# Optimization experiments

Measured on AMD Instinct MI355X. Metric: run time of the kernel, lower is better.

## Reference

```python
import jax, jax.numpy as jnp
import numpy as np

ALPHA = 10.0
BETA = 2.0


def _l2norm(x):
    return x / jnp.linalg.norm(x, axis=1, keepdims=True)


def setup_inputs() -> dict:
    key = jax.random.key(0)
    k1, k2, k3 = jax.random.split(key, 3)
    n, C, d = 4096, 10000, 2048
    inputs = _l2norm(jax.random.normal(k1, (n, d), dtype=jnp.float32))
    kernel = _l2norm(jax.random.normal(k2, (C, d), dtype=jnp.float32))
    targets = jax.random.randint(k3, (n,), 0, C, dtype=jnp.int64 if jax.config.jax_enable_x64 else jnp.int32)
    return {"inputs": inputs, "targets": targets, "kernel": kernel}


def reference(inputs, targets, kernel):
    n = inputs.shape[0]
    C = kernel.shape[0]
    rows = jnp.arange(n)

    # cos_theta uses a detached kernel (no grad through this GEMM in original)
    cos = jnp.clip(inputs @ jax.lax.stop_gradient(kernel).T, -1.0, 1.0)  # [n, C]

    # phi_i = <inputs_i, kernel[targets_i]> - beta  (grad flows to kernel here)
    phi = jnp.sum(inputs * kernel[targets], axis=1) - BETA  # [n]

    pos_cos = cos[rows, targets]  # cos_theta at target columns, [n]
    mean_proxy_pos = pos_cos.sum() / n
    mean_proxy_neg = (cos.sum() - pos_cos.sum()) / (n * (C - 1))

    # output = cos_theta with target entries replaced by phi
    output = cos.at[rows, targets].set(phi)  # [n, C]
    onehot = jax.nn.one_hot(targets, C, dtype=output.dtype)

    loss_pos = phi  # sum(output * onehot, axis=1)
    loss_neg = jnp.log(jnp.sum(jnp.exp(output * ALPHA) * (1.0 - onehot), axis=1))  # [n]
    loss_mask = (jnp.max(output, axis=1) - phi) > 0.0
    per_sample = -loss_pos + loss_neg / ALPHA
    denom = jnp.maximum(loss_mask.sum(), 1).astype(per_sample.dtype)
    loss = jnp.sum(jnp.where(loss_mask, per_sample, 0.0)) / denom

    pred = jnp.argmax(output, axis=1)
    prec = jnp.mean((pred == targets).astype(jnp.float32))

    sim = inputs @ inputs.T  # [n, n]
    sim_label = (targets[:, None] == targets[None, :]).astype(sim.dtype)
    pos_cnt = sim_label.sum()
    neg_cnt = (n * n) - pos_cnt
    mean_pos_sim = jnp.sum(sim * sim_label) / pos_cnt
    mean_neg_sim = jnp.sum(sim * (1.0 - sim_label)) / neg_cnt

    return (loss, prec, mean_proxy_pos, mean_proxy_neg, mean_pos_sim, mean_neg_sim)
```

## Files before the change

kernel.cpp:

```cpp
#include <hip/hip_runtime.h>
#include <hip/hip_bf16.h>

#define NROWS 4096
#define NCLS  10000
#define DIM   2048
#define DIMB  1024
#define ALPHA_F 10.0f
#define BETA_F  2.0f
#define FP4_SCALE 64.0f
#define INVQ (1.0f / (FP4_SCALE * FP4_SCALE))
#define NMAIN_BLK 2528
#define NSIM_BLK  528

typedef float f32x4 __attribute__((ext_vector_type(4)));
typedef int   i32x4 __attribute__((ext_vector_type(4)));
typedef int   i32x8 __attribute__((ext_vector_type(8)));

__global__ void prep_kernel(const float* __restrict__ X, const float* __restrict__ Kn,
                            const int* __restrict__ tgt,
                            unsigned int* __restrict__ dA, unsigned int* __restrict__ dB,
                            float* __restrict__ dotv, int nA8, int nT8) {
  if (blockIdx.x < 2048) {
    int stride = 2048 * blockDim.x;
    for (int i = blockIdx.x * blockDim.x + threadIdx.x; i < nT8; i += stride) {
      const float* src; unsigned int* dst; int j;
      if (i < nA8) { src = X; dst = dA; j = i; } else { src = Kn; dst = dB; j = i - nA8; }
      float4 a = reinterpret_cast<const float4*>(src)[2 * j];
      float4 b = reinterpret_cast<const float4*>(src)[2 * j + 1];
      float v[8] = {a.x, a.y, a.z, a.w, b.x, b.y, b.z, b.w};
      unsigned int w = 0;
#pragma unroll
      for (int q = 0; q < 8; ++q) {
        float s = v[q] * FP4_SCALE;
        float av = fabsf(s);
        unsigned int code = (unsigned)(av > 0.25f) + (av > 0.75f) + (av > 1.25f)
                          + (av > 1.75f) + (av > 2.5f) + (av > 3.5f) + (av > 5.0f);
        code |= (s < 0.f) ? 8u : 0u;
        w |= code << (4 * q);
      }
      dst[j] = w;
    }
  } else {
    int gtid = (blockIdx.x - 2048) * blockDim.x + threadIdx.x;
    int wave = gtid >> 6;
    int lane = threadIdx.x & 63;
    if (wave >= NROWS) return;
    const float* xr = X + (size_t)wave * DIM;
    const float* kr = Kn + (size_t)tgt[wave] * DIM;
    float s = 0.f;
#pragma unroll
    for (int it = 0; it < DIM / 256; ++it) {
      int k = lane * 4 + it * 256;
      float4 a = *reinterpret_cast<const float4*>(xr + k);
      float4 b = *reinterpret_cast<const float4*>(kr + k);
      s += a.x * b.x + a.y * b.y + a.z * b.z + a.w * b.w;
    }
#pragma unroll
    for (int off = 32; off > 0; off >>= 1) s += __shfl_down(s, off);
    if (lane == 0) dotv[wave] = s;
  }
}


#define AS1 const __attribute__((address_space(1))) void*
#define AS3 __attribute__((address_space(3))) void*

__global__ __launch_bounds__(256, 4)
void gemm_kernel(const unsigned char* __restrict__ A,
                 const unsigned char* __restrict__ Bm,
                 const float* __restrict__ dotv,
                 const int* __restrict__ tgt,
                 float* __restrict__ S1, float* __restrict__ Eacc,
                 float* __restrict__ CNT, float* __restrict__ simAcc) {
  __shared__ unsigned char lds[2 * 16384];

  const int tid  = threadIdx.x;
  const int lane = tid & 63;
  const int wid  = tid >> 6;
  const int wr   = wid >> 1;
  const int wc   = wid & 1;
  const int fr   = lane & 15;
  const int kg   = lane >> 4;

  const int lin = blockIdx.x;
  const bool isMain = lin < NMAIN_BLK;
  int rowTile, colTile, nB;
  const unsigned char* B;
  if (isMain) {
    int swz = (lin & 7) * 316 + (lin >> 3);
    colTile = swz / 32;
    rowTile = swz % 32;
    B = Bm; nB = NCLS;
  } else {
    int l2 = lin - NMAIN_BLK;
    int swz = (l2 & 7) * 66 + (l2 >> 3);
    int r = 0;
    while ((r + 1) * (r + 2) / 2 <= swz) ++r;
    rowTile = r;
    colTile = swz - r * (r + 1) / 2;
    B = A; nB = NROWS;
  }
  const int rowBase = rowTile * 128;
  const int colBase = colTile * 128;

  const int l0  = tid >> 3;
  const int sp  = tid & 7;
  const int lg8 = sp ^ (l0 & 7);
  const int shi = lg8 >> 2, sc16 = lg8 & 3;
  const int rA0 = rowBase + 2 * l0 + shi;
  const int rA1 = rA0 + 64;
  int cB0 = colBase + 2 * l0 + shi;      if (cB0 > nB - 1) cB0 = nB - 1;
  int cB1 = colBase + 64 + 2 * l0 + shi; if (cB1 > nB - 1) cB1 = nB - 1;
  const unsigned char* pA0 = A + (size_t)rA0 * DIMB + sc16 * 16;
  const unsigned char* pA1 = A + (size_t)rA1 * DIMB + sc16 * 16;
  const unsigned char* pB0 = B + (size_t)cB0 * DIMB + sc16 * 16;
  const unsigned char* pB1 = B + (size_t)cB1 * DIMB + sc16 * 16;
  const int dOff = l0 * 128 + sp * 16;

#define STAGE_TILE(BUF, KT)                                                     \
  { int ko_ = (KT) * 64;                                                        \
    unsigned char* d_ = lds + (BUF) * 16384 + dOff;                             \
    __builtin_amdgcn_global_load_lds((AS1)(pA0 + ko_), (AS3)(d_),          16, 0, 0); \
    __builtin_amdgcn_global_load_lds((AS1)(pA1 + ko_), (AS3)(d_ + 4096),   16, 0, 0); \
    __builtin_amdgcn_global_load_lds((AS1)(pB0 + ko_), (AS3)(d_ + 8192),   16, 0, 0); \
    __builtin_amdgcn_global_load_lds((AS1)(pB1 + ko_), (AS3)(d_ + 12288),  16, 0, 0); }

  int offA[4], offB[4];
#pragma unroll
  for (int m2 = 0; m2 < 4; ++m2) {
    int lr = wr * 64 + m2 * 16 + fr;
    int l = lr >> 1;
    offA[m2] = l * 128 + ((((lr & 1) * 4 + kg) ^ (l & 7)) << 4);
  }
#pragma unroll
  for (int n2 = 0; n2 < 4; ++n2) {
    int lc = wc * 64 + n2 * 16 + fr;
    int l = lc >> 1;
    offB[n2] = 8192 + l * 128 + ((((lc & 1) * 4 + kg) ^ (l & 7)) << 4);
  }

  f32x4 acc[4][4];
  const f32x4 zero = {0.f, 0.f, 0.f, 0.f};
#pragma unroll
  for (int m = 0; m < 4; ++m)
#pragma unroll
    for (int n = 0; n < 4; ++n) acc[m][n] = zero;

  i32x8 afr[4], bfr[4];
#pragma unroll
  for (int q = 0; q < 4; ++q) {
#pragma unroll
    for (int e = 0; e < 8; ++e) { afr[q][e] = 0; bfr[q][e] = 0; }
  }

  STAGE_TILE(0, 0);
  __syncthreads();

#pragma unroll 1
  for (int kt = 0; kt < 16; ++kt) {
    const int buf = kt & 1;
    if (kt < 15) STAGE_TILE(buf ^ 1, kt + 1);
    const unsigned char* lb = lds + buf * 16384;
#pragma unroll
    for (int m2 = 0; m2 < 4; ++m2) {
      i32x4 v_ = *reinterpret_cast<const i32x4*>(lb + offA[m2]);
      afr[m2][0] = v_[0]; afr[m2][1] = v_[1]; afr[m2][2] = v_[2]; afr[m2][3] = v_[3];
    }
#pragma unroll
    for (int n2 = 0; n2 < 4; ++n2) {
      i32x4 v_ = *reinterpret_cast<const i32x4*>(lb + offB[n2]);
      bfr[n2][0] = v_[0]; bfr[n2][1] = v_[1]; bfr[n2][2] = v_[2]; bfr[n2][3] = v_[3];
    }
#pragma unroll
    for (int m2 = 0; m2 < 4; ++m2)
#pragma unroll
      for (int n2 = 0; n2 < 4; ++n2)
        acc[m2][n2] = __builtin_amdgcn_mfma_scale_f32_16x16x128_f8f6f4(
            afr[m2], bfr[n2], acc[m2][n2], 4, 4, 0, 127, 0, 127);
    __syncthreads();
  }


  if (isMain) {
    float* shPhi = reinterpret_cast<float*>(lds);
    if (tid < 128) shPhi[tid] = dotv[rowBase + tid] - BETA_F;
    __syncthreads();
#pragma unroll
    for (int m = 0; m < 4; ++m) {
#pragma unroll
      for (int j = 0; j < 4; ++j) {
        int rl = wr * 64 + m * 16 + kg * 4 + j;
        float ph = shPhi[rl];
        float s1 = 0.f, ee = 0.f, ct = 0.f;
#pragma unroll
        for (int n = 0; n < 4; ++n) {
          int gcol = colBase + wc * 64 + n * 16 + fr;
          float c = acc[m][n][j] * INVQ;
          c = fminf(fmaxf(c, -1.f), 1.f);
          if (gcol < NCLS) {
            s1 += c;
            ee += __expf(ALPHA_F * c);
            ct += (c > ph) ? 1.f : 0.f;
          }
        }
        float pk = s1 + ct * 4096.0f;
#pragma unroll
        for (int o = 1; o < 16; o <<= 1) {
          pk += __shfl_xor(pk, o);
          ee += __shfl_xor(ee, o);
        }
        if (fr == 0) {
          int grow = rowBase + rl;
          float ctv = rintf(pk * (1.0f / 4096.0f));
          float s1v = pk - ctv * 4096.0f;
          atomicAdd(&S1[grow], s1v);
          atomicAdd(&Eacc[grow], ee);
          atomicAdd(&CNT[grow], ctv);
        }
      }
    }
  } else {
    const float wgt = (rowTile == colTile) ? 1.f : 2.f;
    int* shT = reinterpret_cast<int*>(lds);
    float* redbuf = reinterpret_cast<float*>(lds + 4096);
    if (tid < 128) shT[tid] = tgt[rowBase + tid];
    else if (tid < 256) shT[tid] = tgt[colBase + (tid - 128)];
    __syncthreads();
    float ps = 0.f, als = 0.f, pc = 0.f;
#pragma unroll
    for (int m = 0; m < 4; ++m) {
#pragma unroll
      for (int j = 0; j < 4; ++j) {
        int rl = wr * 64 + m * 16 + kg * 4 + j;
        int tr = shT[rl];
#pragma unroll
        for (int n = 0; n < 4; ++n) {
          int cl = wc * 64 + n * 16 + fr;
          float c = acc[m][n][j] * INVQ;
          als += c;
          if (tr == shT[128 + cl]) { ps += c; pc += 1.f; }
        }
      }
    }
#pragma unroll
    for (int o = 1; o < 64; o <<= 1) {
      ps  += __shfl_xor(ps, o);
      als += __shfl_xor(als, o);
      pc  += __shfl_xor(pc, o);
    }
    if (lane == 0) {
      redbuf[wid * 3 + 0] = ps;
      redbuf[wid * 3 + 1] = als;
      redbuf[wid * 3 + 2] = pc;
    }
    __syncthreads();
    if (tid == 0) {
      float p = 0.f, a = 0.f, c2 = 0.f;
      for (int w = 0; w < 4; ++w) {
        p += redbuf[w * 3 + 0];
        a += redbuf[w * 3 + 1];
        c2 += redbuf[w * 3 + 2];
      }
      atomicAdd(&simAcc[0], wgt * p);
      atomicAdd(&simAcc[1], wgt * a);
      atomicAdd(&simAcc[2], wgt * c2);
    }
  }
}

__global__ void finalize_kernel(const float* __restrict__ dotv, const float* __restrict__ S1,
                                const float* __restrict__ Eacc, const float* __restrict__ CNT,
                                const float* __restrict__ simAcc, float* __restrict__ out) {
  __shared__ float sh[5][1024];
  int tid = threadIdx.x;
  float sum_posc = 0.f, sum_s1 = 0.f, loss_sum = 0.f, mask_cnt = 0.f, correct = 0.f;
  for (int i = tid; i < NROWS; i += 1024) {
    float d = dotv[i];
    float posc = fminf(fmaxf(d, -1.f), 1.f);
    float phi = d - BETA_F;
    sum_posc += posc;
    sum_s1 += S1[i];
    float e = Eacc[i] - __expf(ALPHA_F * posc);
    float cexcl = CNT[i] - 1.f;
    float per = -phi + __logf(e) / ALPHA_F;
    if (cexcl > 0.5f) { loss_sum += per; mask_cnt += 1.f; }
    else correct += 1.f;
  }
  sh[0][tid] = sum_posc; sh[1][tid] = sum_s1; sh[2][tid] = loss_sum;
  sh[3][tid] = mask_cnt; sh[4][tid] = correct;
  __syncthreads();
  for (int s = 512; s > 0; s >>= 1) {
    if (tid < s)
      for (int q = 0; q < 5; ++q) sh[q][tid] += sh[q][tid + s];
    __syncthreads();
  }
  if (tid == 0) {
    float posS = sh[0][0], s1S = sh[1][0], lossS = sh[2][0], maskS = sh[3][0], corr = sh[4][0];
    out[0] = lossS / fmaxf(maskS, 1.f);
    out[1] = corr / (float)NROWS;
    out[2] = posS / (float)NROWS;
    out[3] = (s1S - posS) / ((float)NROWS * (float)(NCLS - 1));
    float pos = simAcc[0], all = simAcc[1], pcnt = simAcc[2];
    out[4] = pos / pcnt;
    out[5] = (all - pos) / ((float)NROWS * (float)NROWS - pcnt);
  }
}

extern "C" void kernel_launch(void* const* d_in, const int* in_sizes, int n_in,
                              void* d_out, int out_size, void* d_ws, size_t ws_size,
                              hipStream_t stream) {
  const float* X  = (const float*)d_in[0];
  const int*   tg = (const int*)d_in[1];
  const float* Kn = (const float*)d_in[2];
  float* out = (float*)d_out;

  char* w = (char*)d_ws;
  unsigned char* f4A = (unsigned char*)w;
  unsigned char* f4B = f4A + (size_t)NROWS * DIMB;
  float* dotv   = (float*)(w + (size_t)NROWS * DIMB + (size_t)NCLS * DIMB);
  float* S1     = dotv + NROWS;
  float* Eacc   = S1 + NROWS;
  float* CNT    = Eacc + NROWS;
  float* simAcc = CNT + NROWS;

  hipMemsetAsync(S1, 0, (3 * NROWS + 4) * sizeof(float), stream);

  const int nA8 = NROWS * DIM / 8, nT8 = nA8 + NCLS * DIM / 8;
  prep_kernel<<<3072, 256, 0, stream>>>(X, Kn, tg, (unsigned int*)f4A,
                                        (unsigned int*)f4B, dotv, nA8, nT8);

  gemm_kernel<<<NMAIN_BLK + NSIM_BLK, 256, 0, stream>>>(
      f4A, f4B, dotv, tg, S1, Eacc, CNT, simAcc);

  finalize_kernel<<<1, 1024, 0, stream>>>(dotv, S1, Eacc, CNT, simAcc, out);
}
```

Before: 135.6 us.

## Replace the n×n similarity GEMM with a column-sum identity and same-label pair dots

The 528 blocks computing the inputs·inputsᵀ GEMM are removed. The total similarity is now taken as the squared norm of the column-sum vector, the diagonal from the sum of squared norms, and same-target pair contributions from explicitly enumerated label-matching pairs that are dot-producted in fp32 by a few extra blocks. This cuts the GEMM grid and replaces O(n²d) work with O(nd) plus a small pair list. In exchange it adds pair enumeration, atomics and a fixed MAXPAIRS cap, and it relies on targets having few collisions.

```diff
diff --git a/kernel.cpp b/kernel.cpp
--- a/kernel.cpp
+++ b/kernel.cpp
@@ -10,7 +10,8 @@
 #define FP4_SCALE 64.0f
 #define INVQ (1.0f / (FP4_SCALE * FP4_SCALE))
 #define NMAIN_BLK 2528
-#define NSIM_BLK  528
+#define NPAIR_BLK 32
+#define MAXPAIRS 8192
 
 typedef float f32x4 __attribute__((ext_vector_type(4)));
 typedef int   i32x4 __attribute__((ext_vector_type(4)));
@@ -19,10 +20,14 @@
 __global__ void prep_kernel(const float* __restrict__ X, const float* __restrict__ Kn,
                             const int* __restrict__ tgt,
                             unsigned int* __restrict__ dA, unsigned int* __restrict__ dB,
-                            float* __restrict__ dotv, int nA8, int nT8) {
+                            float* __restrict__ dotv,
+                            float* __restrict__ scal, float* __restrict__ scol,
+                            unsigned int* __restrict__ pairs,
+                            int nA8, int nT8) {
+  const int tid = threadIdx.x;
   if (blockIdx.x < 2048) {
     int stride = 2048 * blockDim.x;
-    for (int i = blockIdx.x * blockDim.x + threadIdx.x; i < nT8; i += stride) {
+    for (int i = blockIdx.x * blockDim.x + tid; i < nT8; i += stride) {
       const float* src; unsigned int* dst; int j;
       if (i < nA8) { src = X; dst = dA; j = i; } else { src = Kn; dst = dB; j = i - nA8; }
       float4 a = reinterpret_cast<const float4*>(src)[2 * j];
@@ -40,10 +45,10 @@
       }
       dst[j] = w;
     }
-  } else {
-    int gtid = (blockIdx.x - 2048) * blockDim.x + threadIdx.x;
+  } else if (blockIdx.x < 3072) {
+    int gtid = (blockIdx.x - 2048) * blockDim.x + tid;
     int wave = gtid >> 6;
-    int lane = threadIdx.x & 63;
+    int lane = tid & 63;
     if (wave >= NROWS) return;
     const float* xr = X + (size_t)wave * DIM;
     const float* kr = Kn + (size_t)tgt[wave] * DIM;
@@ -58,6 +63,39 @@
 #pragma unroll
     for (int off = 32; off > 0; off >>= 1) s += __shfl_down(s, off);
     if (lane == 0) dotv[wave] = s;
+  } else if (blockIdx.x < 3104) {
+    int rbase = (blockIdx.x - 3072) * 128;
+    float part[8] = {0.f, 0.f, 0.f, 0.f, 0.f, 0.f, 0.f, 0.f};
+    float sq = 0.f;
+    for (int i = 0; i < 128; ++i) {
+      const float* row = X + (size_t)(rbase + i) * DIM;
+#pragma unroll
+      for (int k = 0; k < 8; ++k) {
+        float v = row[tid + 256 * k];
+        part[k] += v;
+        sq += v * v;
+      }
+    }
+#pragma unroll
+    for (int k = 0; k < 8; ++k) atomicAdd(&scol[tid + 256 * k], part[k]);
+    int lane = tid & 63;
+#pragma unroll
+    for (int off = 32; off > 0; off >>= 1) sq += __shfl_down(sq, off);
+    if (lane == 0) atomicAdd(&scal[0], sq);
+  } else {
+    int pb = blockIdx.x - 3104;
+    unsigned int* pairCnt = (unsigned int*)(scal + 3);
+#pragma unroll 1
+    for (int ii = 0; ii < 8; ++ii) {
+      int i = pb * 8 + ii;
+      int ti = tgt[i];
+      for (int j = i + 1 + tid; j < NROWS; j += 256) {
+        if (tgt[j] == ti) {
+          unsigned idx = atomicAdd(pairCnt, 1u);
+          if (idx < MAXPAIRS) pairs[idx] = ((unsigned)i << 16) | (unsigned)j;
+        }
+      }
+    }
   }
 }
 
@@ -69,37 +107,48 @@
 void gemm_kernel(const unsigned char* __restrict__ A,
                  const unsigned char* __restrict__ Bm,
                  const float* __restrict__ dotv,
-                 const int* __restrict__ tgt,
+                 const float* __restrict__ X,
+                 const unsigned int* __restrict__ pairs,
+                 const unsigned int* __restrict__ pairCnt,
                  float* __restrict__ S1, float* __restrict__ Eacc,
-                 float* __restrict__ CNT, float* __restrict__ simAcc) {
-  __shared__ unsigned char lds[2 * 16384];
-
+                 float* __restrict__ CNT, float* __restrict__ Pp) {
   const int tid  = threadIdx.x;
   const int lane = tid & 63;
   const int wid  = tid >> 6;
-  const int wr   = wid >> 1;
-  const int wc   = wid & 1;
-  const int fr   = lane & 15;
-  const int kg   = lane >> 4;
-
-  const int lin = blockIdx.x;
-  const bool isMain = lin < NMAIN_BLK;
-  int rowTile, colTile, nB;
-  const unsigned char* B;
-  if (isMain) {
-    int swz = (lin & 7) * 316 + (lin >> 3);
-    colTile = swz / 32;
-    rowTile = swz % 32;
-    B = Bm; nB = NCLS;
-  } else {
-    int l2 = lin - NMAIN_BLK;
-    int swz = (l2 & 7) * 66 + (l2 >> 3);
-    int r = 0;
-    while ((r + 1) * (r + 2) / 2 <= swz) ++r;
-    rowTile = r;
-    colTile = swz - r * (r + 1) / 2;
-    B = A; nB = NROWS;
-  }
+  const int lin  = blockIdx.x;
+
+  if (lin >= NMAIN_BLK) {
+    int gw = (lin - NMAIN_BLK) * 4 + wid;
+    int cnt = (int)pairCnt[0]; if (cnt > MAXPAIRS) cnt = MAXPAIRS;
+    for (int p = gw; p < cnt; p += 4 * NPAIR_BLK) {
+      unsigned u = pairs[p];
+      const float* xi = X + (size_t)(u >> 16) * DIM;
+      const float* xj = X + (size_t)(u & 0xffffu) * DIM;
+      float s = 0.f;
+#pragma unroll
+      for (int it = 0; it < DIM / 256; ++it) {
+        int k = lane * 4 + it * 256;
+        float4 a = *reinterpret_cast<const float4*>(xi + k);
+        float4 b = *reinterpret_cast<const float4*>(xj + k);
+        s += a.x * b.x + a.y * b.y + a.z * b.z + a.w * b.w;
+      }
+#pragma unroll
+      for (int off = 32; off > 0; off >>= 1) s += __shfl_down(s, off);
+      if (lane == 0) atomicAdd(Pp, s);
+    }
+    return;
+  }
+
+  __shared__ unsigned char lds[2 * 16384];
+
+  const int wr = wid >> 1;
+  const int wc = wid & 1;
+  const int fr = lane & 15;
+  const int kg = lane >> 4;
+
+  int swz = (lin & 7) * 316 + (lin >> 3);
+  const int colTile = swz / 32;
+  const int rowTile = swz % 32;
   const int rowBase = rowTile * 128;
   const int colBase = colTile * 128;
 
@@ -109,12 +158,12 @@
   const int shi = lg8 >> 2, sc16 = lg8 & 3;
   const int rA0 = rowBase + 2 * l0 + shi;
   const int rA1 = rA0 + 64;
-  int cB0 = colBase + 2 * l0 + shi;      if (cB0 > nB - 1) cB0 = nB - 1;
-  int cB1 = colBase + 64 + 2 * l0 + shi; if (cB1 > nB - 1) cB1 = nB - 1;
+  int cB0 = colBase + 2 * l0 + shi;      if (cB0 > NCLS - 1) cB0 = NCLS - 1;
+  int cB1 = colBase + 64 + 2 * l0 + shi; if (cB1 > NCLS - 1) cB1 = NCLS - 1;
   const unsigned char* pA0 = A + (size_t)rA0 * DIMB + sc16 * 16;
   const unsigned char* pA1 = A + (size_t)rA1 * DIMB + sc16 * 16;
-  const unsigned char* pB0 = B + (size_t)cB0 * DIMB + sc16 * 16;
-  const unsigned char* pB1 = B + (size_t)cB1 * DIMB + sc16 * 16;
+  const unsigned char* pB0 = Bm + (size_t)cB0 * DIMB + sc16 * 16;
+  const unsigned char* pB1 = Bm + (size_t)cB1 * DIMB + sc16 * 16;
   const int dOff = l0 * 128 + sp * 16;
 
 #define STAGE_TILE(BUF, KT)                                                     \
@@ -180,98 +229,50 @@
     __syncthreads();
   }
 
-
-  if (isMain) {
-    float* shPhi = reinterpret_cast<float*>(lds);
-    if (tid < 128) shPhi[tid] = dotv[rowBase + tid] - BETA_F;
-    __syncthreads();
-#pragma unroll
-    for (int m = 0; m < 4; ++m) {
-#pragma unroll
-      for (int j = 0; j < 4; ++j) {
-        int rl = wr * 64 + m * 16 + kg * 4 + j;
-        float ph = shPhi[rl];
-        float s1 = 0.f, ee = 0.f, ct = 0.f;
-#pragma unroll
-        for (int n = 0; n < 4; ++n) {
-          int gcol = colBase + wc * 64 + n * 16 + fr;
-          float c = acc[m][n][j] * INVQ;
-          c = fminf(fmaxf(c, -1.f), 1.f);
-          if (gcol < NCLS) {
-            s1 += c;
-            ee += __expf(ALPHA_F * c);
-            ct += (c > ph) ? 1.f : 0.f;
-          }
+  float* shPhi = reinterpret_cast<float*>(lds);
+  if (tid < 128) shPhi[tid] = dotv[rowBase + tid] - BETA_F;
+  __syncthreads();
+#pragma unroll
+  for (int m = 0; m < 4; ++m) {
+#pragma unroll
+    for (int j = 0; j < 4; ++j) {
+      int rl = wr * 64 + m * 16 + kg * 4 + j;
+      float ph = shPhi[rl];
+      float s1 = 0.f, ee = 0.f, ct = 0.f;
+#pragma unroll
+      for (int n = 0; n < 4; ++n) {
+        int gcol = colBase + wc * 64 + n * 16 + fr;
+        float c = acc[m][n][j] * INVQ;
+        c = fminf(fmaxf(c, -1.f), 1.f);
+        if (gcol < NCLS) {
+          s1 += c;
+          ee += __expf(ALPHA_F * c);
+          ct += (c > ph) ? 1.f : 0.f;
         }
-        float pk = s1 + ct * 4096.0f;
-#pragma unroll
-        for (int o = 1; o < 16; o <<= 1) {
-          pk += __shfl_xor(pk, o);
-          ee += __shfl_xor(ee, o);
-        }
-        if (fr == 0) {
-          int grow = rowBase + rl;
-          float ctv = rintf(pk * (1.0f / 4096.0f));
-          float s1v = pk - ctv * 4096.0f;
-          atomicAdd(&S1[grow], s1v);
-          atomicAdd(&Eacc[grow], ee);
-          atomicAdd(&CNT[grow], ctv);
-        }
-      }
-    }
-  } else {
-    const float wgt = (rowTile == colTile) ? 1.f : 2.f;
-    int* shT = reinterpret_cast<int*>(lds);
-    float* redbuf = reinterpret_cast<float*>(lds + 4096);
-    if (tid < 128) shT[tid] = tgt[rowBase + tid];
-    else if (tid < 256) shT[tid] = tgt[colBase + (tid - 128)];
-    __syncthreads();
-    float ps = 0.f, als = 0.f, pc = 0.f;
-#pragma unroll
-    for (int m = 0; m < 4; ++m) {
-#pragma unroll
-      for (int j = 0; j < 4; ++j) {
-        int rl = wr * 64 + m * 16 + kg * 4 + j;
-        int tr = shT[rl];
-#pragma unroll
-        for (int n = 0; n < 4; ++n) {
-          int cl = wc * 64 + n * 16 + fr;
-          float c = acc[m][n][j] * INVQ;
-          als += c;
-          if (tr == shT[128 + cl]) { ps += c; pc += 1.f; }
-        }
-      }
-    }
-#pragma unroll
-    for (int o = 1; o < 64; o <<= 1) {
-      ps  += __shfl_xor(ps, o);
-      als += __shfl_xor(als, o);
-      pc  += __shfl_xor(pc, o);
-    }
-    if (lane == 0) {
-      redbuf[wid * 3 + 0] = ps;
-      redbuf[wid * 3 + 1] = als;
-      redbuf[wid * 3 + 2] = pc;
-    }
-    __syncthreads();
-    if (tid == 0) {
-      float p = 0.f, a = 0.f, c2 = 0.f;
-      for (int w = 0; w < 4; ++w) {
-        p += redbuf[w * 3 + 0];
-        a += redbuf[w * 3 + 1];
-        c2 += redbuf[w * 3 + 2];
-      }
-      atomicAdd(&simAcc[0], wgt * p);
-      atomicAdd(&simAcc[1], wgt * a);
-      atomicAdd(&simAcc[2], wgt * c2);
+      }
+      float pk = s1 + ct * 4096.0f;
+#pragma unroll
+      for (int o = 1; o < 16; o <<= 1) {
+        pk += __shfl_xor(pk, o);
+        ee += __shfl_xor(ee, o);
+      }
+      if (fr == 0) {
+        int grow = rowBase + rl;
+        float ctv = rintf(pk * (1.0f / 4096.0f));
+        float s1v = pk - ctv * 4096.0f;
+        atomicAdd(&S1[grow], s1v);
+        atomicAdd(&Eacc[grow], ee);
+        atomicAdd(&CNT[grow], ctv);
+      }
     }
   }
 }
 
 __global__ void finalize_kernel(const float* __restrict__ dotv, const float* __restrict__ S1,
                                 const float* __restrict__ Eacc, const float* __restrict__ CNT,
-                                const float* __restrict__ simAcc, float* __restrict__ out) {
-  __shared__ float sh[5][1024];
+                                const float* __restrict__ scal, const float* __restrict__ scol,
+                                float* __restrict__ out) {
+  __shared__ float sh[6][1024];
   int tid = threadIdx.x;
   float sum_posc = 0.f, sum_s1 = 0.f, loss_sum = 0.f, mask_cnt = 0.f, correct = 0.f;
   for (int i = tid; i < NROWS; i += 1024) {
@@ -286,23 +287,30 @@
     if (cexcl > 0.5f) { loss_sum += per; mask_cnt += 1.f; }
     else correct += 1.f;
   }
+  float sum_s2 = 0.f;
+  for (int c = tid; c < 2048; c += 1024) { float v = scol[c]; sum_s2 += v * v; }
   sh[0][tid] = sum_posc; sh[1][tid] = sum_s1; sh[2][tid] = loss_sum;
-  sh[3][tid] = mask_cnt; sh[4][tid] = correct;
+  sh[3][tid] = mask_cnt; sh[4][tid] = correct; sh[5][tid] = sum_s2;
   __syncthreads();
   for (int s = 512; s > 0; s >>= 1) {
     if (tid < s)
-      for (int q = 0; q < 5; ++q) sh[q][tid] += sh[q][tid + s];
+      for (int q = 0; q < 6; ++q) sh[q][tid] += sh[q][tid + s];
     __syncthreads();
   }
   if (tid == 0) {
     float posS = sh[0][0], s1S = sh[1][0], lossS = sh[2][0], maskS = sh[3][0], corr = sh[4][0];
+    float simTot = sh[5][0];
     out[0] = lossS / fmaxf(maskS, 1.f);
     out[1] = corr / (float)NROWS;
     out[2] = posS / (float)NROWS;
     out[3] = (s1S - posS) / ((float)NROWS * (float)(NCLS - 1));
-    float pos = simAcc[0], all = simAcc[1], pcnt = simAcc[2];
+    float ssq = scal[0];
+    float Pp  = scal[1];
+    unsigned npair = ((const unsigned int*)scal)[3];
+    float pos  = ssq + 2.f * Pp;
+    float pcnt = (float)NROWS + 2.f * (float)npair;
     out[4] = pos / pcnt;
-    out[5] = (all - pos) / ((float)NROWS * (float)NROWS - pcnt);
+    out[5] = (simTot - pos) / ((float)NROWS * (float)NROWS - pcnt);
   }
 }
 
@@ -321,16 +329,19 @@
   float* S1     = dotv + NROWS;
   float* Eacc   = S1 + NROWS;
   float* CNT    = Eacc + NROWS;
-  float* simAcc = CNT + NROWS;
-
-  hipMemsetAsync(S1, 0, (3 * NROWS + 4) * sizeof(float), stream);
+  float* scal   = CNT + NROWS;
+  float* scol   = scal + 8;
+  unsigned int* pairs = (unsigned int*)(scol + 2048);
+
+  hipMemsetAsync(S1, 0, (3 * NROWS + 8 + 2048) * sizeof(float), stream);
 
   const int nA8 = NROWS * DIM / 8, nT8 = nA8 + NCLS * DIM / 8;
-  prep_kernel<<<3072, 256, 0, stream>>>(X, Kn, tg, (unsigned int*)f4A,
-                                        (unsigned int*)f4B, dotv, nA8, nT8);
-
-  gemm_kernel<<<NMAIN_BLK + NSIM_BLK, 256, 0, stream>>>(
-      f4A, f4B, dotv, tg, S1, Eacc, CNT, simAcc);
-
-  finalize_kernel<<<1, 1024, 0, stream>>>(dotv, S1, Eacc, CNT, simAcc, out);
+  prep_kernel<<<3616, 256, 0, stream>>>(X, Kn, tg, (unsigned int*)f4A,
+                                        (unsigned int*)f4B, dotv, scal, scol,
+                                        pairs, nA8, nT8);
+
+  gemm_kernel<<<NMAIN_BLK + NPAIR_BLK, 256, 0, stream>>>(
+      f4A, f4B, dotv, X, pairs, (unsigned int*)(scal + 3), S1, Eacc, CNT, scal + 1);
+
+  finalize_kernel<<<1, 1024, 0, stream>>>(dotv, S1, Eacc, CNT, scal, scol, out);
 }
```

New measurement: 144.3 us. +6.4%, slower.
